# Optimization experiments

Measured on AMD Instinct MI355X. Metric: run time of the kernel, lower is better.

The kernel has to match this reference:

```python
import jax, jax.numpy as jnp
import numpy as np

B, N, NUM = 16384, 512, 3  # batch, num queries, num vanishing points per image


def setup_inputs() -> dict:
    key = jax.random.key(0)
    k1, k2, k3 = jax.random.split(key, 3)
    pred_logits = jax.random.normal(k1, (B, N, 1), jnp.float32)
    pp = jax.random.normal(k2, (B, N, 3), jnp.float32)
    pred_pos = pp / jnp.linalg.norm(pp, axis=-1, keepdims=True)  # unit directions
    vp = jax.random.normal(k3, (B, 3, NUM), jnp.float32)
    vps_unique = vp / jnp.linalg.norm(vp, axis=1, keepdims=True)  # all columns valid (abs-sum > 1e-5)
    return {"pred_logits": pred_logits, "pred_pos": pred_pos, "vps_unique": vps_unique}


def _greedy_select(conf, pos, num):
    # conf: [N,1], pos: [N,3]; greedy angular NMS keeping `num` candidates.
    order = jnp.argsort(-conf[:, 0]).astype(jnp.int32)  # descending confidence
    thresh = jnp.pi / (num + 1)
    ar = jnp.arange(num)
    cand0 = jnp.zeros((num,), jnp.int32).at[0].set(order[0])

    def step(carry, idx):
        cand, count = carry
        sel = pos[cand]                                   # [num,3]
        dots = jnp.minimum(jnp.abs(sel @ pos[idx]), 1.0)  # clip for arccos stability
        ang = jnp.where(ar < count, jnp.arccos(dots), jnp.inf)
        add = (count < num) & (jnp.min(ang) >= thresh)    # torch: skip if dst < pi/(num+1)
        cand = jnp.where(add & (ar == count), idx, cand)
        return (cand, count + add.astype(jnp.int32)), None

    (cand, _), _ = jax.lax.scan(step, (cand0, jnp.int32(1)), order[1:])
    return pos[cand]  # [num,3]


def reference(pred_logits, pred_pos, vps_unique):
    num = vps_unique.shape[2]  # static: all vps columns are valid by construction
    sel = jax.vmap(lambda c, p: _greedy_select(c, p, num))(pred_logits, pred_pos)
    return sel  # [B, num, 3]
```

## Files before the change

### kernel.cpp

```cpp
#include <hip/hip_runtime.h>
#include <math.h>

#define B_TOTAL 16384
#define NQ 512
#define NUM 3

typedef unsigned u32;

__device__ __forceinline__ u32 wave_umax_dpp(u32 v) {
    u32 r = v, t;
    t = (u32)__builtin_amdgcn_update_dpp(0, (int)r, 0x111, 0xF, 0xF, false);
    r = t > r ? t : r;
    t = (u32)__builtin_amdgcn_update_dpp(0, (int)r, 0x112, 0xF, 0xF, false);
    r = t > r ? t : r;
    t = (u32)__builtin_amdgcn_update_dpp(0, (int)r, 0x114, 0xF, 0xF, false);
    r = t > r ? t : r;
    t = (u32)__builtin_amdgcn_update_dpp(0, (int)r, 0x118, 0xF, 0xF, false);
    r = t > r ? t : r;
    t = (u32)__builtin_amdgcn_update_dpp(0, (int)r, 0x142, 0xF, 0xF, false);
    r = t > r ? t : r;
    t = (u32)__builtin_amdgcn_update_dpp(0, (int)r, 0x143, 0xF, 0xF, false);
    r = t > r ? t : r;
    return (u32)__builtin_amdgcn_readlane((int)r, 63);
}

__device__ __forceinline__ u32 wave_umin_dpp(u32 v) {
    u32 r = v, t;
    t = (u32)__builtin_amdgcn_update_dpp(-1, (int)r, 0x111, 0xF, 0xF, false);
    r = t < r ? t : r;
    t = (u32)__builtin_amdgcn_update_dpp(-1, (int)r, 0x112, 0xF, 0xF, false);
    r = t < r ? t : r;
    t = (u32)__builtin_amdgcn_update_dpp(-1, (int)r, 0x114, 0xF, 0xF, false);
    r = t < r ? t : r;
    t = (u32)__builtin_amdgcn_update_dpp(-1, (int)r, 0x118, 0xF, 0xF, false);
    r = t < r ? t : r;
    t = (u32)__builtin_amdgcn_update_dpp(-1, (int)r, 0x142, 0xF, 0xF, false);
    r = t < r ? t : r;
    t = (u32)__builtin_amdgcn_update_dpp(-1, (int)r, 0x143, 0xF, 0xF, false);
    r = t < r ? t : r;
    return (u32)__builtin_amdgcn_readlane((int)r, 63);
}

__global__ __launch_bounds__(256) void greedy_nms_kernel(
    const float* __restrict__ conf,
    const float* __restrict__ pos,
    float* __restrict__ out)
{
    const int lane = threadIdx.x & 63;
    const int b = (blockIdx.x << 2) | (threadIdx.x >> 6);

    const float* cb = conf + (size_t)b * NQ;
    const float* pb = pos  + (size_t)b * NQ * 3;

    const float4* cb4 = reinterpret_cast<const float4*>(cb);
    const float4 c0 = cb4[lane * 2 + 0];
    const float4 c1 = cb4[lane * 2 + 1];
    const float p0x = pb[0], p0y = pb[1], p0z = pb[2];

    u32 k[8];
    {
        float f[8] = {c0.x, c0.y, c0.z, c0.w, c1.x, c1.y, c1.z, c1.w};
        #pragma unroll
        for (int s = 0; s < 8; ++s) {
            int bi = __float_as_int(f[s]);
            k[s] = (u32)bi ^ ((u32)(bi >> 31) | 0x80000000u);
        }
    }

    auto argmax_dpp = [&](u32& gm_out) -> int {
        u32 m = k[0];
        #pragma unroll
        for (int s = 1; s < 8; ++s) m = k[s] > m ? k[s] : m;
        const u32 gm = wave_umax_dpp(m);
        int im = 8;
        #pragma unroll
        for (int s = 7; s >= 0; --s)
            if (k[s] == gm) im = s;
        const u32 candn = (im < 8) ? (u32)((lane << 3) | im) : 0xFFFFFFFFu;
        const u32 n = wave_umin_dpp(candn);
        gm_out = gm;
        return (int)n;
    };

    auto consume = [&](int n) {
        const int ci = ((n >> 3) == lane) ? (n & 7) : 8;
        #pragma unroll
        for (int s = 0; s < 8; ++s)
            if (ci == s) k[s] = 0u;
    };

    const float TH  = 0.78539816339744830961f;
    const float CLO = 0.70710478f;
    const float CHI = 0.70710878f;

    auto passv = [&](float ax, float ay, float az,
                     float px, float py, float pz) -> bool {
        float d = fabsf(ax * px + ay * py + az * pz);
        if (d <= CLO) return true;
        if (d >= CHI) return false;
        return acosf(fminf(d, 1.f)) >= TH;
    };

    u32 gm1;
    const int w1 = argmax_dpp(gm1);
    consume(w1);
    const float p1x = pb[w1 * 3 + 0];
    const float p1y = pb[w1 * 3 + 1];
    const float p1z = pb[w1 * 3 + 2];

    float a1x = 0.f, a1y = 0.f, a1z = 0.f;
    float o2x = p0x, o2y = p0y, o2z = p0z;
    float o3x = p0x, o3y = p0y, o3z = p0z;
    int count = 1;

    #pragma unroll 1
    for (int it = 1; it < NQ; ++it) {
        u32 gm;
        const int n = argmax_dpp(gm);
        if (gm == 0u) break;
        consume(n);
        const float px = pb[n * 3 + 0];
        const float py = pb[n * 3 + 1];
        const float pz = pb[n * 3 + 2];
        const bool add = passv(p1x, p1y, p1z, px, py, pz) &&
                         passv(a1x, a1y, a1z, px, py, pz);
        if (add) {
            if (count == 1) {
                o2x = px; o2y = py; o2z = pz;
                a1x = px; a1y = py; a1z = pz;
                count = 2;
            } else {
                o3x = px; o3y = py; o3z = pz;
                break;
            }
        }
    }

    if (lane == 0) {
        float* ob = out + (size_t)b * 9;
        ob[0] = p1x; ob[1] = p1y; ob[2] = p1z;
        ob[3] = o2x; ob[4] = o2y; ob[5] = o2z;
        ob[6] = o3x; ob[7] = o3y; ob[8] = o3z;
    }
}

extern "C" void kernel_launch(void* const* d_in, const int* in_sizes, int n_in,
                              void* d_out, int out_size, void* d_ws, size_t ws_size,
                              hipStream_t stream) {
    const float* pred_logits = (const float*)d_in[0];
    const float* pred_pos    = (const float*)d_in[1];
    float* out = (float*)d_out;

    const int grid = B_TOTAL / 4;
    greedy_nms_kernel<<<grid, 256, 0, stream>>>(pred_logits, pred_pos, out);
}
```

Measured before the change: 26.45 us.

## Process two batch items per wave to interleave independent greedy NMS chains

Each wave now handles two images (b and b+8192) and runs their argmax/consume/test loops interleaved, halving the grid. The goal is to overlap the latency-bound serial DPP reductions and dependent position loads of two independent chains, giving more instruction-level parallelism per wave. In exchange it uses more registers and adds branching on per-item run flags, and a wave keeps running until its slower item finishes.

```diff
diff --git a/kernel.cpp b/kernel.cpp
--- a/kernel.cpp
+++ b/kernel.cpp
@@ -4,6 +4,7 @@
 #define B_TOTAL 16384
 #define NQ 512
 #define NUM 3
+#define NWAVES 8192
 
 typedef unsigned u32;
 
@@ -47,27 +48,34 @@
     float* __restrict__ out)
 {
     const int lane = threadIdx.x & 63;
-    const int b = (blockIdx.x << 2) | (threadIdx.x >> 6);
-
-    const float* cb = conf + (size_t)b * NQ;
-    const float* pb = pos  + (size_t)b * NQ * 3;
-
-    const float4* cb4 = reinterpret_cast<const float4*>(cb);
-    const float4 c0 = cb4[lane * 2 + 0];
-    const float4 c1 = cb4[lane * 2 + 1];
-    const float p0x = pb[0], p0y = pb[1], p0z = pb[2];
-
-    u32 k[8];
+    const int wg = (blockIdx.x << 2) | (threadIdx.x >> 6);
+    const int bA = wg;
+    const int bB = wg + NWAVES;
+
+    const float* pbA = pos + (size_t)bA * NQ * 3;
+    const float* pbB = pos + (size_t)bB * NQ * 3;
+
+    const float4* cA4 = reinterpret_cast<const float4*>(conf + (size_t)bA * NQ);
+    const float4* cB4 = reinterpret_cast<const float4*>(conf + (size_t)bB * NQ);
+    const float4 a0 = cA4[lane * 2 + 0];
+    const float4 a1 = cA4[lane * 2 + 1];
+    const float4 b0 = cB4[lane * 2 + 0];
+    const float4 b1 = cB4[lane * 2 + 1];
+
+    u32 kA[8], kB[8];
     {
-        float f[8] = {c0.x, c0.y, c0.z, c0.w, c1.x, c1.y, c1.z, c1.w};
+        float fA[8] = {a0.x, a0.y, a0.z, a0.w, a1.x, a1.y, a1.z, a1.w};
+        float fB[8] = {b0.x, b0.y, b0.z, b0.w, b1.x, b1.y, b1.z, b1.w};
         #pragma unroll
         for (int s = 0; s < 8; ++s) {
-            int bi = __float_as_int(f[s]);
-            k[s] = (u32)bi ^ ((u32)(bi >> 31) | 0x80000000u);
-        }
-    }
-
-    auto argmax_dpp = [&](u32& gm_out) -> int {
+            int ia = __float_as_int(fA[s]);
+            kA[s] = (u32)ia ^ ((u32)(ia >> 31) | 0x80000000u);
+            int ib = __float_as_int(fB[s]);
+            kB[s] = (u32)ib ^ ((u32)(ib >> 31) | 0x80000000u);
+        }
+    }
+
+    auto argmax_dpp = [&](u32 (&k)[8], u32& gm_out) -> int {
         u32 m = k[0];
         #pragma unroll
         for (int s = 1; s < 8; ++s) m = k[s] > m ? k[s] : m;
@@ -82,7 +90,7 @@
         return (int)n;
     };
 
-    auto consume = [&](int n) {
+    auto consume = [&](u32 (&k)[8], int n) {
         const int ci = ((n >> 3) == lane) ? (n & 7) : 8;
         #pragma unroll
         for (int s = 0; s < 8; ++s)
@@ -101,46 +109,107 @@
         return acosf(fminf(d, 1.f)) >= TH;
     };
 
-    u32 gm1;
-    const int w1 = argmax_dpp(gm1);
-    consume(w1);
-    const float p1x = pb[w1 * 3 + 0];
-    const float p1y = pb[w1 * 3 + 1];
-    const float p1z = pb[w1 * 3 + 2];
-
-    float a1x = 0.f, a1y = 0.f, a1z = 0.f;
-    float o2x = p0x, o2y = p0y, o2z = p0z;
-    float o3x = p0x, o3y = p0y, o3z = p0z;
-    int count = 1;
+    u32 g;
+    const int w1A = argmax_dpp(kA, g); consume(kA, w1A);
+    const int w1B = argmax_dpp(kB, g); consume(kB, w1B);
+    const float p1Ax = pbA[w1A * 3 + 0];
+    const float p1Ay = pbA[w1A * 3 + 1];
+    const float p1Az = pbA[w1A * 3 + 2];
+    const float p1Bx = pbB[w1B * 3 + 0];
+    const float p1By = pbB[w1B * 3 + 1];
+    const float p1Bz = pbB[w1B * 3 + 2];
+
+    float a1Ax = 0.f, a1Ay = 0.f, a1Az = 0.f;
+    float a1Bx = 0.f, a1By = 0.f, a1Bz = 0.f;
+    float o2Ax = 0.f, o2Ay = 0.f, o2Az = 0.f;
+    float o2Bx = 0.f, o2By = 0.f, o2Bz = 0.f;
+    int cntA = 1, cntB = 1;
+    bool runA = true, runB = true;
 
     #pragma unroll 1
-    for (int it = 1; it < NQ; ++it) {
-        u32 gm;
-        const int n = argmax_dpp(gm);
-        if (gm == 0u) break;
-        consume(n);
-        const float px = pb[n * 3 + 0];
-        const float py = pb[n * 3 + 1];
-        const float pz = pb[n * 3 + 2];
-        const bool add = passv(p1x, p1y, p1z, px, py, pz) &&
-                         passv(a1x, a1y, a1z, px, py, pz);
-        if (add) {
-            if (count == 1) {
-                o2x = px; o2y = py; o2z = pz;
-                a1x = px; a1y = py; a1z = pz;
-                count = 2;
-            } else {
-                o3x = px; o3y = py; o3z = pz;
-                break;
+    for (int it = 1; it < NQ && (runA || runB); ++it) {
+        int nA = 0, nB = 0;
+        u32 gmA = 0u, gmB = 0u;
+        if (runA) nA = argmax_dpp(kA, gmA);
+        if (runB) nB = argmax_dpp(kB, gmB);
+        const bool actA = runA && (gmA != 0u);
+        const bool actB = runB && (gmB != 0u);
+        if (runA && gmA == 0u) runA = false;
+        if (runB && gmB == 0u) runB = false;
+
+        float pAx, pAy, pAz, pBx, pBy, pBz;
+        if (actA) {
+            consume(kA, nA);
+            pAx = pbA[nA * 3 + 0]; pAy = pbA[nA * 3 + 1]; pAz = pbA[nA * 3 + 2];
+        }
+        if (actB) {
+            consume(kB, nB);
+            pBx = pbB[nB * 3 + 0]; pBy = pbB[nB * 3 + 1]; pBz = pbB[nB * 3 + 2];
+        }
+
+        if (actA) {
+            const bool add = passv(p1Ax, p1Ay, p1Az, pAx, pAy, pAz) &&
+                             passv(a1Ax, a1Ay, a1Az, pAx, pAy, pAz);
+            if (add) {
+                if (cntA == 1) {
+                    o2Ax = pAx; o2Ay = pAy; o2Az = pAz;
+                    a1Ax = pAx; a1Ay = pAy; a1Az = pAz;
+                    cntA = 2;
+                } else {
+                    if (lane == 0) {
+                        float* ob = out + (size_t)bA * 9;
+                        ob[0] = p1Ax; ob[1] = p1Ay; ob[2] = p1Az;
+                        ob[3] = o2Ax; ob[4] = o2Ay; ob[5] = o2Az;
+                        ob[6] = pAx;  ob[7] = pAy;  ob[8] = pAz;
+                    }
+                    cntA = 3; runA = false;
+                }
             }
         }
-    }
-
-    if (lane == 0) {
-        float* ob = out + (size_t)b * 9;
-        ob[0] = p1x; ob[1] = p1y; ob[2] = p1z;
-        ob[3] = o2x; ob[4] = o2y; ob[5] = o2z;
-        ob[6] = o3x; ob[7] = o3y; ob[8] = o3z;
+        if (actB) {
+            const bool add = passv(p1Bx, p1By, p1Bz, pBx, pBy, pBz) &&
+                             passv(a1Bx, a1By, a1Bz, pBx, pBy, pBz);
+            if (add) {
+                if (cntB == 1) {
+                    o2Bx = pBx; o2By = pBy; o2Bz = pBz;
+                    a1Bx = pBx; a1By = pBy; a1Bz = pBz;
+                    cntB = 2;
+                } else {
+                    if (lane == 0) {
+                        float* ob = out + (size_t)bB * 9;
+                        ob[0] = p1Bx; ob[1] = p1By; ob[2] = p1Bz;
+                        ob[3] = o2Bx; ob[4] = o2By; ob[5] = o2Bz;
+                        ob[6] = pBx;  ob[7] = pBy;  ob[8] = pBz;
+                    }
+                    cntB = 3; runB = false;
+                }
+            }
+        }
+    }
+
+    if (cntA < 3) {
+        const float p0x = pbA[0], p0y = pbA[1], p0z = pbA[2];
+        const float q2x = (cntA >= 2) ? o2Ax : p0x;
+        const float q2y = (cntA >= 2) ? o2Ay : p0y;
+        const float q2z = (cntA >= 2) ? o2Az : p0z;
+        if (lane == 0) {
+            float* ob = out + (size_t)bA * 9;
+            ob[0] = p1Ax; ob[1] = p1Ay; ob[2] = p1Az;
+            ob[3] = q2x;  ob[4] = q2y;  ob[5] = q2z;
+            ob[6] = p0x;  ob[7] = p0y;  ob[8] = p0z;
+        }
+    }
+    if (cntB < 3) {
+        const float p0x = pbB[0], p0y = pbB[1], p0z = pbB[2];
+        const float q2x = (cntB >= 2) ? o2Bx : p0x;
+        const float q2y = (cntB >= 2) ? o2By : p0y;
+        const float q2z = (cntB >= 2) ? o2Bz : p0z;
+        if (lane == 0) {
+            float* ob = out + (size_t)bB * 9;
+            ob[0] = p1Bx; ob[1] = p1By; ob[2] = p1Bz;
+            ob[3] = q2x;  ob[4] = q2y;  ob[5] = q2z;
+            ob[6] = p0x;  ob[7] = p0y;  ob[8] = p0z;
+        }
     }
 }
 
@@ -151,6 +220,5 @@
     const float* pred_pos    = (const float*)d_in[1];
     float* out = (float*)d_out;
 
-    const int grid = B_TOTAL / 4;
-    greedy_nms_kernel<<<grid, 256, 0, stream>>>(pred_logits, pred_pos, out);
-}
+    greedy_nms_kernel<<<NWAVES / 4, 256, 0, stream>>>(pred_logits, pred_pos, out);
+}
```

Measured after the change: 31.89 us. 20.5% more time.

## Pre-extract top-8 candidates and resolve greedy NMS with wave ballots

Applied to the files above, without the earlier changes.

Replaces the DPP min-reduction in argmax with a ballot plus find-first-set and readlane to locate the lowest owning lane. Pulls the top 8 candidates up front, one per lane, then uses two ballots of the angular test to pick the second and third selections in parallel. The serial per-candidate loop only runs as a fallback when fewer than three survivors appear among the top 8. This cuts the serial dependent reduction chain per step, at the cost of always doing 8 argmax rounds.

```diff
diff --git a/kernel.cpp b/kernel.cpp
--- a/kernel.cpp
+++ b/kernel.cpp
@@ -4,8 +4,10 @@
 #define B_TOTAL 16384
 #define NQ 512
 #define NUM 3
+#define TOPK 8
 
 typedef unsigned u32;
+typedef unsigned long long u64;
 
 __device__ __forceinline__ u32 wave_umax_dpp(u32 v) {
     u32 r = v, t;
@@ -24,21 +26,8 @@
     return (u32)__builtin_amdgcn_readlane((int)r, 63);
 }
 
-__device__ __forceinline__ u32 wave_umin_dpp(u32 v) {
-    u32 r = v, t;
-    t = (u32)__builtin_amdgcn_update_dpp(-1, (int)r, 0x111, 0xF, 0xF, false);
-    r = t < r ? t : r;
-    t = (u32)__builtin_amdgcn_update_dpp(-1, (int)r, 0x112, 0xF, 0xF, false);
-    r = t < r ? t : r;
-    t = (u32)__builtin_amdgcn_update_dpp(-1, (int)r, 0x114, 0xF, 0xF, false);
-    r = t < r ? t : r;
-    t = (u32)__builtin_amdgcn_update_dpp(-1, (int)r, 0x118, 0xF, 0xF, false);
-    r = t < r ? t : r;
-    t = (u32)__builtin_amdgcn_update_dpp(-1, (int)r, 0x142, 0xF, 0xF, false);
-    r = t < r ? t : r;
-    t = (u32)__builtin_amdgcn_update_dpp(-1, (int)r, 0x143, 0xF, 0xF, false);
-    r = t < r ? t : r;
-    return (u32)__builtin_amdgcn_readlane((int)r, 63);
+__device__ __forceinline__ float bcastf(float v, int l) {
+    return __int_as_float(__builtin_amdgcn_readlane(__float_as_int(v), l));
 }
 
 __global__ __launch_bounds__(256) void greedy_nms_kernel(
@@ -55,7 +44,6 @@
     const float4* cb4 = reinterpret_cast<const float4*>(cb);
     const float4 c0 = cb4[lane * 2 + 0];
     const float4 c1 = cb4[lane * 2 + 1];
-    const float p0x = pb[0], p0y = pb[1], p0z = pb[2];
 
     u32 k[8];
     {
@@ -67,7 +55,7 @@
         }
     }
 
-    auto argmax_dpp = [&](u32& gm_out) -> int {
+    auto argmax_fast = [&](u32& gm_out) -> int {
         u32 m = k[0];
         #pragma unroll
         for (int s = 1; s < 8; ++s) m = k[s] > m ? k[s] : m;
@@ -76,10 +64,11 @@
         #pragma unroll
         for (int s = 7; s >= 0; --s)
             if (k[s] == gm) im = s;
-        const u32 candn = (im < 8) ? (u32)((lane << 3) | im) : 0xFFFFFFFFu;
-        const u32 n = wave_umin_dpp(candn);
+        const u64 ball = __ballot(im < 8);
+        const int owner = __ffsll(ball) - 1;
+        const int oim = __builtin_amdgcn_readlane(im, owner);
         gm_out = gm;
-        return (int)n;
+        return (owner << 3) | oim;
     };
 
     auto consume = [&](int n) {
@@ -88,6 +77,19 @@
         for (int s = 0; s < 8; ++s)
             if (ci == s) k[s] = 0u;
     };
+
+    float gx = 0.f, gy = 0.f, gz = 0.f;
+    #pragma unroll
+    for (int i = 0; i < TOPK; ++i) {
+        u32 gm;
+        const int n = argmax_fast(gm);
+        consume(n);
+        if (lane == i) {
+            gx = pb[n * 3 + 0];
+            gy = pb[n * 3 + 1];
+            gz = pb[n * 3 + 2];
+        }
+    }
 
     const float TH  = 0.78539816339744830961f;
     const float CLO = 0.70710478f;
@@ -101,22 +103,43 @@
         return acosf(fminf(d, 1.f)) >= TH;
     };
 
-    u32 gm1;
-    const int w1 = argmax_dpp(gm1);
-    consume(w1);
-    const float p1x = pb[w1 * 3 + 0];
-    const float p1y = pb[w1 * 3 + 1];
-    const float p1z = pb[w1 * 3 + 2];
+    const float p1x = bcastf(gx, 0), p1y = bcastf(gy, 0), p1z = bcastf(gz, 0);
+    const u64 ball1 = __ballot(passv(p1x, p1y, p1z, gx, gy, gz)) & 0xFEull;
 
+    float o2x, o2y, o2z;
+    bool have2 = false;
+    if (ball1 != 0) {
+        const int i2 = __ffsll(ball1) - 1;
+        o2x = bcastf(gx, i2); o2y = bcastf(gy, i2); o2z = bcastf(gz, i2);
+        have2 = true;
+        const u64 ball3 = ball1 & __ballot(passv(o2x, o2y, o2z, gx, gy, gz))
+                                & ~((2ull << i2) - 1);
+        if (ball3 != 0) {
+            const int i3 = __ffsll(ball3) - 1;
+            const float o3x = bcastf(gx, i3);
+            const float o3y = bcastf(gy, i3);
+            const float o3z = bcastf(gz, i3);
+            if (lane == 0) {
+                float* ob = out + (size_t)b * 9;
+                ob[0] = p1x; ob[1] = p1y; ob[2] = p1z;
+                ob[3] = o2x; ob[4] = o2y; ob[5] = o2z;
+                ob[6] = o3x; ob[7] = o3y; ob[8] = o3z;
+            }
+            return;
+        }
+    }
+
+    const float p0x = pb[0], p0y = pb[1], p0z = pb[2];
     float a1x = 0.f, a1y = 0.f, a1z = 0.f;
-    float o2x = p0x, o2y = p0y, o2z = p0z;
     float o3x = p0x, o3y = p0y, o3z = p0z;
     int count = 1;
+    if (have2) { a1x = o2x; a1y = o2y; a1z = o2z; count = 2; }
+    else       { o2x = p0x; o2y = p0y; o2z = p0z; }
 
     #pragma unroll 1
-    for (int it = 1; it < NQ; ++it) {
+    for (int it = TOPK; it < NQ; ++it) {
         u32 gm;
-        const int n = argmax_dpp(gm);
+        const int n = argmax_fast(gm);
         if (gm == 0u) break;
         consume(n);
         const float px = pb[n * 3 + 0];
```

New measurement: 28.51 us. 7.8% more time.
